# Performance work log

Hardware: AMD Instinct MI355X
Metric: run time of the kernel (lower is better)

The kernel has to match this reference:

```python
import jax, jax.numpy as jnp
import numpy as np

D = 384      # d_model
DM = 256     # memory feature dim
DF = 1536    # dim_feedforward
EPS = 1e-5


def _layer_norm(x, g, b):
    m = jnp.mean(x, axis=-1, keepdims=True)
    v = jnp.mean(jnp.square(x - m), axis=-1, keepdims=True)
    return (x - m) * jax.lax.rsqrt(v + EPS) * g + b


def setup_inputs() -> dict:
    key = jax.random.key(0)
    ks = jax.random.split(key, 24)
    B, T, T1, Tc = 8, 2048, 2048, 2048
    s = 0.02
    inp = {
        "tgt": jax.random.normal(ks[0], (B, T, D), jnp.float32),
        "memory": jax.random.normal(ks[1], (B, T1, DM), jnp.float32),
        "a1": jnp.float32(0.5),
        "score_c": jax.random.normal(ks[2], (B, 1, Tc, T1), jnp.float32) * 0.1,
        "out_c": jax.random.normal(ks[3], (B, Tc, D), jnp.float32),
        # attention projections
        "Wq": jax.random.normal(ks[4], (D, D), jnp.float32) * s,
        "bq": jnp.zeros((D,), jnp.float32),
        "Wk": jax.random.normal(ks[5], (DM, D), jnp.float32) * s,
        "bk": jnp.zeros((D,), jnp.float32),
        "Wv": jax.random.normal(ks[6], (DM, D), jnp.float32) * s,
        "bv": jnp.zeros((D,), jnp.float32),
        "Wu": jax.random.normal(ks[7], (D, D), jnp.float32) * s,  # unknown
        "bu": jnp.zeros((D,), jnp.float32),
        "Wn": jax.random.normal(ks[8], (D, D), jnp.float32) * s,  # known
        "bn": jnp.zeros((D,), jnp.float32),
        # FFN
        "W1": jax.random.normal(ks[9], (D, DF), jnp.float32) * s,
        "b1": jnp.zeros((DF,), jnp.float32),
        "W2": jax.random.normal(ks[10], (DF, D), jnp.float32) * s,
        "b2": jnp.zeros((D,), jnp.float32),
        # LayerNorms
        "g1": jnp.ones((D,), jnp.float32),
        "be1": jnp.zeros((D,), jnp.float32),
        "g2": jnp.ones((D,), jnp.float32),
        "be2": jnp.zeros((D,), jnp.float32),
    }
    return inp


def reference(tgt, memory, a1, score_c, out_c,
              Wq, bq, Wk, bk, Wv, bv, Wu, bu, Wn, bn,
              W1, b1, W2, b2, g1, be1, g2, be2):
    # --- En_De_Attention (n_head = 1; dropout p=0 / eval mode -> identity) ---
    scale = 1.0 / jnp.sqrt(jnp.float32(D))
    q = tgt @ Wq + bq                  # [B,T,D]
    k = memory @ Wk + bk               # [B,T1,D]
    v = memory @ Wv + bv               # [B,T1,D]
    att = jnp.einsum('btd,bsd->bts', q, k) * scale            # [B,T,T1]

    unknow = tgt @ Wu + bu             # [B,T,D]
    know = out_c @ Wn + bn             # [B,Tc,D]
    score1 = jnp.einsum('btd,bcd->btc', unknow, know) * scale  # [B,T,Tc]
    mixed = jnp.einsum('btc,bcs->bts', score1, score_c[:, 0])  # [B,T,T1]

    # tt = a1 in (0,1]: blended-score branch of the original module
    score = a1 * jax.nn.softmax(mixed, axis=-1) \
          + (1.0 - a1) * jax.nn.softmax(att, axis=-1)          # [B,T,T1]
    z = jnp.einsum('bts,bsd->btd', score, v)                   # [B,T,D]

    # --- residual + norm1 ---
    x = _layer_norm(tgt + z, g1, be1)
    # --- FFN (relu) + residual + norm2 (dropout eval -> identity) ---
    ff = jax.nn.relu(x @ W1 + b1) @ W2 + b2
    out = _layer_norm(x + ff, g2, be2)
    # score2 returned with head dim, matching torch shape [B,1,T,T1]
    return out, score[:, None]
```

## Files before the change

### kernel.cpp

```cpp
#include <hip/hip_runtime.h>
#include <stdint.h>

typedef __attribute__((ext_vector_type(8))) short bf16x8;
typedef __attribute__((ext_vector_type(4))) float f32x4;

__device__ __forceinline__ short f2bf(float f) {
    union { float f; unsigned u; } v; v.f = f;
    unsigned r = v.u + 0x7fffu + ((v.u >> 16) & 1u);
    return (short)(r >> 16);
}
__device__ __forceinline__ float bf2f(short s) {
    union { unsigned u; float f; } v;
    v.u = ((unsigned)(unsigned short)s) << 16;
    return v.f;
}

__device__ __forceinline__ void gld16(const void* g, void* l) {
    auto gp = reinterpret_cast<const __attribute__((address_space(1))) unsigned int*>(
        reinterpret_cast<uintptr_t>(g));
    auto lp = reinterpret_cast<__attribute__((address_space(3))) unsigned int*>(
        reinterpret_cast<uintptr_t>(l));
    __builtin_amdgcn_global_load_lds(gp, lp, 16, 0, 0);
}

template<int OUTBF, int BIASMODE , int DORELU>
__global__ __launch_bounds__(256, 3) void gemm128r(
    const short* __restrict__ Ag, const short* __restrict__ Bg,
    void* __restrict__ Cg, const float* __restrict__ bias,
    int K, int lda, int ldb, int ldc,
    long long sA, long long sB, long long sC,
    long long dA, long long dB, long long dC, float scale)
{
    __shared__ short lds[3 * 8192];
    const int t = threadIdx.x;
    const int lane = t & 63;
    const int wave = t >> 6;
    const int wm = wave >> 1, wn = wave & 1;

    const int gx = gridDim.x, gy = gridDim.y;
    const int nwg = gx * gy * gridDim.z;
    int id = blockIdx.x + gx * (blockIdx.y + gy * blockIdx.z);
    id = (id & 7) * (nwg >> 3) + (id >> 3);
    const int bx = id % gx;
    const int by = (id / gx) % gy;
    const int bz = id / (gx * gy);
    const int zlo = bz & 7, zhi = bz >> 3;

    const long long row0 = (long long)by * 128;
    const long long col0 = (long long)bx * 128;
    const int NT = K >> 5;

    const int gk = ((t & 3) ^ ((t >> 2) & 3) ^ ((t >> 4) & 3)) * 8;
    const short* Asrc = Ag + zlo * sA + zhi * dA + (row0 + (t >> 2)) * (long long)lda + gk;
    const short* Bsrc = Bg + zlo * sB + zhi * dB + (col0 + (t >> 2)) * (long long)ldb + gk;

    const int frow = lane & 15;
    const int fcol = ((lane >> 4) ^ (frow & 3) ^ ((frow >> 2) & 3)) * 8;

    f32x4 acc[4][4] = {};

#define STG(BUF, KC) do { \
        gld16(Asrc + (KC), &lds[(BUF) * 8192 + t * 8]); \
        gld16(Asrc + (KC) + 64LL * lda, &lds[(BUF) * 8192 + 2048 + t * 8]); \
        gld16(Bsrc + (KC), &lds[(BUF) * 8192 + 4096 + t * 8]); \
        gld16(Bsrc + (KC) + 64LL * ldb, &lds[(BUF) * 8192 + 6144 + t * 8]); } while (0)

    STG(0, 0);
    STG(1, 32);
    asm volatile("s_waitcnt vmcnt(4)\ns_barrier" ::: "memory");

    for (int kt = 0; kt < NT; ++kt) {
        const int rb = (kt % 3) * 8192;
        bf16x8 av[4], bv[4];
#pragma unroll
        for (int m = 0; m < 4; ++m)
            av[m] = *(const bf16x8*)&lds[rb + (wm * 64 + m * 16 + frow) * 32 + fcol];
#pragma unroll
        for (int n = 0; n < 4; ++n)
            bv[n] = *(const bf16x8*)&lds[rb + 4096 + (wn * 64 + n * 16 + frow) * 32 + fcol];
        if (kt + 2 < NT) STG((kt + 2) % 3, (long long)(kt + 2) * 32);
        __builtin_amdgcn_s_setprio(1);
#pragma unroll
        for (int m = 0; m < 4; ++m)
#pragma unroll
            for (int n = 0; n < 4; ++n)
                acc[m][n] = __builtin_amdgcn_mfma_f32_16x16x32_bf16(av[m], bv[n], acc[m][n], 0, 0, 0);
        __builtin_amdgcn_s_setprio(0);
        if (kt + 1 < NT) {
            if (kt + 2 < NT) asm volatile("s_waitcnt vmcnt(4)\ns_barrier" ::: "memory");
            else             asm volatile("s_waitcnt vmcnt(0)\ns_barrier" ::: "memory");
        }
    }
#undef STG

    const int crow = (lane >> 4) * 4;
    const int ccol = lane & 15;
    const long long cz = zlo * sC + zhi * dC;
#pragma unroll
    for (int m = 0; m < 4; ++m)
#pragma unroll
        for (int n = 0; n < 4; ++n)
#pragma unroll
            for (int i = 0; i < 4; ++i) {
                long long r = row0 + wm * 64 + m * 16 + crow + i;
                long long c = col0 + wn * 64 + n * 16 + ccol;
                float v = acc[m][n][i] * scale;
                if (BIASMODE == 1) v += bias[c];
                if (BIASMODE == 2) v += bias[r];
                if (DORELU) v = fmaxf(v, 0.0f);
                long long idx = cz + r * (long long)ldc + c;
                if (OUTBF) ((short*)Cg)[idx] = f2bf(v);
                else ((float*)Cg)[idx] = v;
            }
}

#define RD_A(RB, M, KS) (*(const bf16x8*)&lds[(RB) + (wm * 64 + (M) * 16 + frow) * 64 + \
        ((((KS) << 2) | fq) ^ (frow & 7)) * 8])
#define RD_B(RB, Nn, KS) (*(const bf16x8*)&lds[(RB) + 8192 + (wn * 64 + (Nn) * 16 + frow) * 64 + \
        ((((KS) << 2) | fq) ^ (frow & 7)) * 8])

__global__ __launch_bounds__(256, 2) void gemm128pz(
    const short* __restrict__ A1, const short* __restrict__ B1, short* __restrict__ C1,
    const float* __restrict__ bias1, int K1, int lda1, int ldb1, int ldc1,
    long long sB1, long long sC1,
    const short* __restrict__ A2, const short* __restrict__ B2, short* __restrict__ C2,
    const float* __restrict__ bias2, int K2, int lda2, int ldb2, int ldc2,
    long long sB2, long long sC2)
{
    __shared__ short lds[2 * 16384];
    const int t = threadIdx.x;
    const int lane = t & 63;
    const int wave = t >> 6;
    const int wm = wave >> 1, wn = wave & 1;

    const int gx = gridDim.x, gy = gridDim.y;
    const int nwg = gx * gy * gridDim.z;
    int id = blockIdx.x + gx * (blockIdx.y + gy * blockIdx.z);
    id = (id & 7) * (nwg >> 3) + (id >> 3);
    const int bx = id % gx;
    const int by = (id / gx) % gy;
    const int bz = id / (gx * gy);

    const bool sel = bz >= 8;
    const int zz = bz & 7;
    const short* Ag = sel ? A2 : A1;
    const short* Bg = sel ? B2 : B1;
    short* Cg = sel ? C2 : C1;
    const float* bias = sel ? bias2 : bias1;
    const int K = sel ? K2 : K1;
    const int lda = sel ? lda2 : lda1;
    const int ldb = sel ? ldb2 : ldb1;
    const int ldc = sel ? ldc2 : ldc1;
    const long long sB = sel ? sB2 : sB1;
    const long long sC = sel ? sC2 : sC1;

    const long long row0 = (long long)by * 128;
    const long long col0 = (long long)bx * 128;
    const int NT = K >> 6;

    const int srow = t >> 3;
    const int gk = ((t & 7) ^ (srow & 7)) * 8;
    const short* Asrc = Ag + (row0 + srow) * (long long)lda + gk;
    const short* Bsrc = Bg + (long long)zz * sB + (col0 + srow) * (long long)ldb + gk;

    const int frow = lane & 15;
    const int fq = lane >> 4;

    f32x4 acc[4][4] = {};

#define STAGE_A(WB, KC) do { _Pragma("unroll") \
        for (int r = 0; r < 4; ++r) \
            gld16(Asrc + (KC) + (long long)r * 32 * lda, &lds[(WB) + t * 8 + r * 2048]); } while (0)
#define STAGE_B(WB, KC) do { _Pragma("unroll") \
        for (int r = 0; r < 4; ++r) \
            gld16(Bsrc + (KC) + (long long)r * 32 * ldb, &lds[(WB) + 8192 + t * 8 + r * 2048]); } while (0)

    STAGE_A(0, 0);
    STAGE_B(0, 0);
    asm volatile("s_waitcnt vmcnt(0)\ns_barrier" ::: "memory");

    for (int kt = 0; kt < NT; ++kt) {
        const int rb = (kt & 1) << 14;
        const int wb = ((kt + 1) & 1) << 14;
        const bool st = (kt + 1) < NT;
        const long long kc = (long long)(kt + 1) << 6;

        bf16x8 av[4], bv[4];

#pragma unroll
        for (int m = 0; m < 4; ++m) av[m] = RD_A(rb, m, 0);
#pragma unroll
        for (int n = 0; n < 4; ++n) bv[n] = RD_B(rb, n, 0);
        if (st) STAGE_A(wb, kc);
        asm volatile("s_barrier" ::: "memory");
        __builtin_amdgcn_s_setprio(1);
#pragma unroll
        for (int m = 0; m < 4; ++m)
#pragma unroll
            for (int n = 0; n < 4; ++n)
                acc[m][n] = __builtin_amdgcn_mfma_f32_16x16x32_bf16(av[m], bv[n], acc[m][n], 0, 0, 0);
        __builtin_amdgcn_s_setprio(0);
        asm volatile("s_barrier" ::: "memory");

#pragma unroll
        for (int m = 0; m < 4; ++m) av[m] = RD_A(rb, m, 1);
#pragma unroll
        for (int n = 0; n < 4; ++n) bv[n] = RD_B(rb, n, 1);
        if (st) STAGE_B(wb, kc);
        asm volatile("s_barrier" ::: "memory");
        __builtin_amdgcn_s_setprio(1);
#pragma unroll
        for (int m = 0; m < 4; ++m)
#pragma unroll
            for (int n = 0; n < 4; ++n)
                acc[m][n] = __builtin_amdgcn_mfma_f32_16x16x32_bf16(av[m], bv[n], acc[m][n], 0, 0, 0);
        __builtin_amdgcn_s_setprio(0);
        if (st) asm volatile("s_waitcnt vmcnt(0)\ns_barrier" ::: "memory");
        else    asm volatile("s_barrier" ::: "memory");
    }
#undef STAGE_A
#undef STAGE_B

    const int crow = (lane >> 4) * 4;
    const int ccol = lane & 15;
    const long long cz = (long long)zz * sC;
#pragma unroll
    for (int m = 0; m < 4; ++m)
#pragma unroll
        for (int n = 0; n < 4; ++n)
#pragma unroll
            for (int i = 0; i < 4; ++i) {
                long long r = row0 + wm * 64 + m * 16 + crow + i;
                long long c = col0 + wn * 64 + n * 16 + ccol;
                float v = acc[m][n][i] + bias[r];
                Cg[cz + r * (long long)ldc + c] = f2bf(v);
            }
}
#undef RD_A
#undef RD_B

__global__ __launch_bounds__(256) void cast_all(
    const float* __restrict__ tgt, const float* __restrict__ mem, const float* __restrict__ outc,
    const float* __restrict__ bq, const float* __restrict__ bu,
    short* __restrict__ tgtb, short* __restrict__ memb, short* __restrict__ outcb,
    float* __restrict__ qubias)
{
    const long long R1 = 1572864;
    const long long R2 = R1 + 1048576;
    const long long R3 = R2 + 1572864;
    const long long R4 = R3 + 192;
    long long i = (long long)blockIdx.x * 256 + threadIdx.x;
    const float* in; short* out; long long j;
    if (i < R1) { in = tgt; out = tgtb; j = i; }
    else if (i < R2) { in = mem; out = memb; j = i - R1; }
    else if (i < R3) { in = outc; out = outcb; j = i - R2; }
    else if (i < R4) {
        j = i - R3;
        ((float4*)qubias)[j] = (j < 96) ? ((const float4*)bq)[j] : ((const float4*)bu)[j - 96];
        return;
    } else return;
    float4 v = ((const float4*)in)[j];
    short4 o;
    o.x = f2bf(v.x); o.y = f2bf(v.y); o.z = f2bf(v.z); o.w = f2bf(v.w);
    ((short4*)out)[j] = o;
}

__global__ __launch_bounds__(256) void transpose_all(
    const float* __restrict__ Wq, const float* __restrict__ Wk, const float* __restrict__ Wv,
    const float* __restrict__ Wu, const float* __restrict__ Wn,
    const float* __restrict__ W1, const float* __restrict__ W2,
    short* __restrict__ WquT, short* __restrict__ WkT, short* __restrict__ WvT,
    short* __restrict__ WnT, short* __restrict__ W1T, short* __restrict__ W2T)
{
    __shared__ float tile[64][65];
    int b = blockIdx.x;
    const float* in; short* out; int R, C, local;
    if (b < 36)       { in = Wq; out = WquT;          R = 384;  C = 384;  local = b; }
    else if (b < 60)  { in = Wk; out = WkT;           R = 256;  C = 384;  local = b - 36; }
    else if (b < 84)  { in = Wv; out = WvT;           R = 256;  C = 384;  local = b - 60; }
    else if (b < 120) { in = Wu; out = WquT + 147456; R = 384;  C = 384;  local = b - 84; }
    else if (b < 156) { in = Wn; out = WnT;           R = 384;  C = 384;  local = b - 120; }
    else if (b < 300) { in = W1; out = W1T;           R = 384;  C = 1536; local = b - 156; }
    else              { in = W2; out = W2T;           R = 1536; C = 384;  local = b - 300; }
    const int nbx = C >> 6;
    const int r0 = (local / nbx) * 64, c0 = (local % nbx) * 64;
    const int lr = threadIdx.x >> 6, lc = threadIdx.x & 63;
#pragma unroll
    for (int i = 0; i < 16; ++i) {
        int r = lr * 16 + i;
        tile[r][lc] = in[(long long)(r0 + r) * C + c0 + lc];
    }
    __syncthreads();
#pragma unroll
    for (int i = 0; i < 16; ++i) {
        int r = lr * 16 + i;
        out[(long long)(c0 + r) * R + r0 + lc] = f2bf(tile[lc][r]);
    }
}

__global__ __launch_bounds__(256) void transpose_cast(
    const float* __restrict__ in, short* __restrict__ out,
    int R, int C, long long sIn, long long sOut)
{
    __shared__ float tile[64][65];
    const long long zi = (long long)blockIdx.z * sIn;
    const long long zo = (long long)blockIdx.z * sOut;
    const int r0 = blockIdx.y * 64, c0 = blockIdx.x * 64;
    const int lr = threadIdx.x >> 6, lc = threadIdx.x & 63;
#pragma unroll
    for (int i = 0; i < 16; ++i) {
        int r = lr * 16 + i;
        tile[r][lc] = in[zi + (long long)(r0 + r) * C + c0 + lc];
    }
    __syncthreads();
#pragma unroll
    for (int i = 0; i < 16; ++i) {
        int r = lr * 16 + i;
        out[zo + (long long)(c0 + r) * R + r0 + lc] = f2bf(tile[lc][r]);
    }
}

__global__ __launch_bounds__(256) void softmax_blend(
    const short* __restrict__ attb, const short* __restrict__ mixb,
    const float* __restrict__ a1p,
    float* __restrict__ outF, short* __restrict__ outB)
{
    const int S = 2048;
    const long long row = blockIdx.x;
    const short* ar = attb + row * S;
    const short* mr = mixb + row * S;
    const int t = threadIdx.x;
    const int wave = t >> 6;

    bf16x8 a8 = *(const bf16x8*)&ar[t * 8];
    bf16x8 m8 = *(const bf16x8*)&mr[t * 8];
    float av[8], mv[8];
#pragma unroll
    for (int i = 0; i < 8; ++i) { av[i] = bf2f(a8[i]); mv[i] = bf2f(m8[i]); }

    float amax = av[0], mmax = mv[0];
#pragma unroll
    for (int i = 1; i < 8; ++i) { amax = fmaxf(amax, av[i]); mmax = fmaxf(mmax, mv[i]); }
#pragma unroll
    for (int o = 32; o; o >>= 1) {
        amax = fmaxf(amax, __shfl_xor(amax, o));
        mmax = fmaxf(mmax, __shfl_xor(mmax, o));
    }
    __shared__ float red[2][4];
    if ((t & 63) == 0) { red[0][wave] = amax; red[1][wave] = mmax; }
    __syncthreads();
    amax = fmaxf(fmaxf(red[0][0], red[0][1]), fmaxf(red[0][2], red[0][3]));
    mmax = fmaxf(fmaxf(red[1][0], red[1][1]), fmaxf(red[1][2], red[1][3]));

    float asum = 0.f, msum = 0.f;
#pragma unroll
    for (int i = 0; i < 8; ++i) {
        av[i] = __expf(av[i] - amax); asum += av[i];
        mv[i] = __expf(mv[i] - mmax); msum += mv[i];
    }
#pragma unroll
    for (int o = 32; o; o >>= 1) {
        asum += __shfl_xor(asum, o);
        msum += __shfl_xor(msum, o);
    }
    __shared__ float red2[2][4];
    if ((t & 63) == 0) { red2[0][wave] = asum; red2[1][wave] = msum; }
    __syncthreads();
    asum = red2[0][0] + red2[0][1] + red2[0][2] + red2[0][3];
    msum = red2[1][0] + red2[1][1] + red2[1][2] + red2[1][3];

    const float a1 = a1p[0];
    const float wm = a1 / msum;
    const float wa = (1.0f - a1) / asum;

    float o0[8];
    bf16x8 ob;
#pragma unroll
    for (int i = 0; i < 8; ++i) {
        float s = wm * mv[i] + wa * av[i];
        o0[i] = s;
        ob[i] = f2bf(s);
    }
    float4 f0, f1;
    f0.x = o0[0]; f0.y = o0[1]; f0.z = o0[2]; f0.w = o0[3];
    f1.x = o0[4]; f1.y = o0[5]; f1.z = o0[6]; f1.w = o0[7];
    *(float4*)&outF[row * S + t * 8] = f0;
    *(float4*)&outF[row * S + t * 8 + 4] = f1;
    *(bf16x8*)&outB[row * S + t * 8] = ob;
}

template<int WRITE_BF>
__global__ __launch_bounds__(256) void ln_kernel(
    const float* __restrict__ X, const float* __restrict__ Yr,
    const float* __restrict__ g, const float* __restrict__ be,
    float* __restrict__ outF, short* __restrict__ outB)
{
    const int Dm = 384;
    const int wave = threadIdx.x >> 6, lane = threadIdx.x & 63;
    const long long row = (long long)blockIdx.x * 4 + wave;
    const float* x = X + row * Dm;
    const float* y = Yr + row * Dm;
    float h[6];
    float s = 0.f, s2 = 0.f;
#pragma unroll
    for (int j = 0; j < 6; ++j) {
        int c = j * 64 + lane;
        h[j] = x[c] + y[c];
        s += h[j]; s2 += h[j] * h[j];
    }
#pragma unroll
    for (int o = 32; o; o >>= 1) { s += __shfl_xor(s, o); s2 += __shfl_xor(s2, o); }
    const float mean = s * (1.0f / 384.0f);
    const float var = s2 * (1.0f / 384.0f) - mean * mean;
    const float rstd = rsqrtf(var + 1e-5f);
#pragma unroll
    for (int j = 0; j < 6; ++j) {
        int c = j * 64 + lane;
        float v = (h[j] - mean) * rstd * g[c] + be[c];
        outF[row * Dm + c] = v;
        if (WRITE_BF) outB[row * Dm + c] = f2bf(v);
    }
}

extern "C" void kernel_launch(void* const* d_in, const int* in_sizes, int n_in,
                              void* d_out, int out_size, void* d_ws, size_t ws_size,
                              hipStream_t stream) {
    const float* tgt     = (const float*)d_in[0];
    const float* memory  = (const float*)d_in[1];
    const float* a1      = (const float*)d_in[2];
    const float* score_c = (const float*)d_in[3];
    const float* out_c   = (const float*)d_in[4];
    const float* Wq = (const float*)d_in[5];  const float* bq = (const float*)d_in[6];
    const float* Wk = (const float*)d_in[7];  const float* bk = (const float*)d_in[8];
    const float* Wv = (const float*)d_in[9];  const float* bv = (const float*)d_in[10];
    const float* Wu = (const float*)d_in[11]; const float* bu = (const float*)d_in[12];
    const float* Wn = (const float*)d_in[13]; const float* bn = (const float*)d_in[14];
    const float* W1 = (const float*)d_in[15]; const float* b1 = (const float*)d_in[16];
    const float* W2 = (const float*)d_in[17]; const float* b2 = (const float*)d_in[18];
    const float* g1 = (const float*)d_in[19]; const float* be1 = (const float*)d_in[20];
    const float* g2 = (const float*)d_in[21]; const float* be2 = (const float*)d_in[22];

    const long long BT = 16384;
    const long long S2 = 2048LL * 2048;
    const long long PB = 2048LL * 384;
    char* ws = (char*)d_ws;
    size_t off = 0;
    auto A_ = [&](size_t b) { size_t r = off; off += (b + 255) & ~(size_t)255; return r; };

    const size_t oTgtB  = A_(BT * 384 * 2);
    const size_t oMemB  = A_(BT * 256 * 2);
    const size_t oOutcB = A_(BT * 384 * 2);
    const size_t oWquT  = A_(768 * 384 * 2);
    const size_t oWnT   = A_(384 * 384 * 2);
    const size_t oWkT   = A_(384 * 256 * 2);
    const size_t oWvT   = A_(384 * 256 * 2);
    const size_t oW1T   = A_(1536 * 384 * 2);
    const size_t oW2T   = A_(384 * 1536 * 2);
    const size_t oQUb   = A_(768 * 4);
    const size_t oQU    = A_(16 * PB * 2);
    const size_t oKP    = A_(16 * PB * 2);
    const size_t oVT    = A_(8LL * 384 * 2048 * 2);
    const size_t oJ     = A_(8 * S2 * 2);
    const size_t oKr    = A_(8 * S2 * 2);
    const size_t oAM    = A_(16 * S2 * 2);
    const size_t oX     = A_(BT * 384 * 4);
    const size_t oXB    = A_(BT * 384 * 2);

    short* tgt_bf  = (short*)(ws + oTgtB);
    short* mem_bf  = (short*)(ws + oMemB);
    short* outc_bf = (short*)(ws + oOutcB);
    short* WquT = (short*)(ws + oWquT);
    short* WnT  = (short*)(ws + oWnT);
    short* WkT  = (short*)(ws + oWkT);
    short* WvT  = (short*)(ws + oWvT);
    short* W1T  = (short*)(ws + oW1T);
    short* W2T  = (short*)(ws + oW2T);
    float* qu_bias = (float*)(ws + oQUb);
    short* qu_bf  = (short*)(ws + oQU);
    short* k_bf   = (short*)(ws + oKP);
    short* Pt_bf  = k_bf + 8 * PB;
    short* vT_bf  = (short*)(ws + oVT);
    short* score_bf = (short*)(ws + oJ);
    short* scoreCt  = (short*)(ws + oKr);
    float* z_f      = (float*)(ws + oKr);
    short* knoT_bf  = (short*)(ws + oAM);
    short* att_bf   = (short*)(ws + oAM);
    short* mix_bf   = att_bf + 8 * S2;
    short* h_bf     = (short*)(ws + oAM);
    float* ff_f     = (float*)(ws + oAM + 8 * S2 * 2);
    float* x_f  = (float*)(ws + oX);
    short* x_bf = (short*)(ws + oXB);

    float* outMain = (float*)d_out;
    float* outScore = (float*)d_out + 6291456;

    const float SC = 0.05103103630798288f;
    dim3 blk(256);

    cast_all<<<16385, blk, 0, stream>>>(tgt, memory, out_c, bq, bu,
                                        tgt_bf, mem_bf, outc_bf, qu_bias);
    transpose_all<<<444, blk, 0, stream>>>(Wq, Wk, Wv, Wu, Wn, W1, W2,
                                           WquT, WkT, WvT, WnT, W1T, W2T);
    transpose_cast<<<dim3(32, 32, 8), blk, 0, stream>>>(score_c, scoreCt, 2048, 2048, S2, S2);

    gemm128r<1, 1, 0><<<dim3(6, 128, 1), blk, 0, stream>>>(
        tgt_bf, WquT, qu_bf, qu_bias, 384, 384, 384, 768, 0, 0, 0, 0, 0, 0, 1.0f);
    gemm128r<1, 1, 0><<<dim3(3, 128, 1), blk, 0, stream>>>(
        mem_bf, WkT, k_bf, bk, 256, 256, 256, 384, 0, 0, 0, 0, 0, 0, 1.0f);
    gemm128pz<<<dim3(16, 3, 16), blk, 0, stream>>>(
        WvT, mem_bf, vT_bf, bv, 256, 256, 256, 2048, 2048LL * 256, PB,
        WnT, outc_bf, knoT_bf, bn, 384, 384, 384, 2048, PB, PB);
    gemm128r<1, 0, 0><<<dim3(3, 16, 8), blk, 0, stream>>>(
        scoreCt, knoT_bf, Pt_bf, nullptr, 2048, 2048, 2048, 384,
        S2, PB, PB, 0, 0, 0, 1.0f);
    gemm128r<1, 0, 0><<<dim3(16, 16, 16), blk, 0, stream>>>(
        qu_bf, k_bf, att_bf, nullptr, 384, 768, 384, 2048,
        2048LL * 768, PB, S2, 384, 8 * PB, 8 * S2, SC);
    softmax_blend<<<16384, blk, 0, stream>>>(att_bf, mix_bf, a1, outScore, score_bf);
    gemm128r<0, 0, 0><<<dim3(3, 16, 8), blk, 0, stream>>>(
        score_bf, vT_bf, z_f, nullptr, 2048, 2048, 2048, 384,
        S2, PB, PB, 0, 0, 0, 1.0f);
    ln_kernel<1><<<4096, blk, 0, stream>>>(tgt, z_f, g1, be1, x_f, x_bf);
    gemm128r<1, 1, 1><<<dim3(12, 128, 1), blk, 0, stream>>>(
        x_bf, W1T, h_bf, b1, 384, 384, 384, 1536, 0, 0, 0, 0, 0, 0, 1.0f);
    gemm128r<0, 1, 0><<<dim3(3, 128, 1), blk, 0, stream>>>(
        h_bf, W2T, ff_f, b2, 1536, 1536, 1536, 384, 0, 0, 0, 0, 0, 0, 1.0f);
    ln_kernel<0><<<4096, blk, 0, stream>>>(x_f, ff_f, g2, be2, outMain, nullptr);
}
```

Before: 456.3 us.

## Add 128x256 wide-tile GEMM and split-K the score·V GEMM

Measured after the change: 866.8 us. 1.9x slower.

```diff
diff --git a/kernel.cpp b/kernel.cpp
--- a/kernel.cpp
+++ b/kernel.cpp
@@ -21,6 +21,98 @@
     auto lp = reinterpret_cast<__attribute__((address_space(3))) unsigned int*>(
         reinterpret_cast<uintptr_t>(l));
     __builtin_amdgcn_global_load_lds(gp, lp, 16, 0, 0);
+}
+
+template<int OUTBF, int BIASMODE , int DORELU>
+__global__ __launch_bounds__(256, 2) void gemmWide(
+    const short* __restrict__ Ag, const short* __restrict__ Bg,
+    void* __restrict__ Cg, const float* __restrict__ bias,
+    int K, int lda, int ldb, int ldc,
+    long long sA, long long sB, long long sC,
+    long long dA, long long dB, long long dC, float scale)
+{
+    __shared__ short lds[3 * 12288];
+    const int t = threadIdx.x;
+    const int lane = t & 63;
+    const int wave = t >> 6;
+    const int wm = wave >> 1, wn = wave & 1;
+
+    const int gx = gridDim.x, gy = gridDim.y;
+    const int nwg = gx * gy * gridDim.z;
+    int id = blockIdx.x + gx * (blockIdx.y + gy * blockIdx.z);
+    id = (id & 7) * (nwg >> 3) + (id >> 3);
+    const int bx = id % gx;
+    const int by = (id / gx) % gy;
+    const int bz = id / (gx * gy);
+    const int zlo = bz & 7, zhi = bz >> 3;
+
+    const long long row0 = (long long)by * 128;
+    const long long col0 = (long long)bx * 256;
+    const int NT = K >> 5;
+
+    const int gk = ((t & 3) ^ ((t >> 2) & 3) ^ ((t >> 4) & 3)) * 8;
+    const short* Asrc = Ag + zlo * sA + zhi * dA + (row0 + (t >> 2)) * (long long)lda + gk;
+    const short* Bsrc = Bg + zlo * sB + zhi * dB + (col0 + (t >> 2)) * (long long)ldb + gk;
+
+    const int frow = lane & 15;
+    const int fcol = ((lane >> 4) ^ (frow & 3) ^ ((frow >> 2) & 3)) * 8;
+
+    f32x4 acc[4][8] = {};
+
+#define STG(BUF, KC) do { \
+        gld16(Asrc + (KC), &lds[(BUF) * 12288 + t * 8]); \
+        gld16(Asrc + (KC) + 64LL * lda, &lds[(BUF) * 12288 + 2048 + t * 8]); \
+        gld16(Bsrc + (KC), &lds[(BUF) * 12288 + 4096 + t * 8]); \
+        gld16(Bsrc + (KC) + 64LL * ldb, &lds[(BUF) * 12288 + 6144 + t * 8]); \
+        gld16(Bsrc + (KC) + 128LL * ldb, &lds[(BUF) * 12288 + 8192 + t * 8]); \
+        gld16(Bsrc + (KC) + 192LL * ldb, &lds[(BUF) * 12288 + 10240 + t * 8]); } while (0)
+
+    STG(0, 0);
+    STG(1, 32);
+    asm volatile("s_waitcnt vmcnt(6)\ns_barrier" ::: "memory");
+
+    for (int kt = 0; kt < NT; ++kt) {
+        const int rb = (kt % 3) * 12288;
+        bf16x8 av[4], bv[8];
+#pragma unroll
+        for (int m = 0; m < 4; ++m)
+            av[m] = *(const bf16x8*)&lds[rb + (wm * 64 + m * 16 + frow) * 32 + fcol];
+#pragma unroll
+        for (int n = 0; n < 8; ++n)
+            bv[n] = *(const bf16x8*)&lds[rb + 4096 + (wn * 128 + n * 16 + frow) * 32 + fcol];
+        if (kt + 2 < NT) STG((kt + 2) % 3, (long long)(kt + 2) * 32);
+        __builtin_amdgcn_s_setprio(1);
+#pragma unroll
+        for (int m = 0; m < 4; ++m)
+#pragma unroll
+            for (int n = 0; n < 8; ++n)
+                acc[m][n] = __builtin_amdgcn_mfma_f32_16x16x32_bf16(av[m], bv[n], acc[m][n], 0, 0, 0);
+        __builtin_amdgcn_s_setprio(0);
+        if (kt + 1 < NT) {
+            if (kt + 2 < NT) asm volatile("s_waitcnt vmcnt(6)\ns_barrier" ::: "memory");
+            else             asm volatile("s_waitcnt vmcnt(0)\ns_barrier" ::: "memory");
+        }
+    }
+#undef STG
+
+    const int crow = (lane >> 4) * 4;
+    const int ccol = lane & 15;
+    const long long cz = zlo * sC + zhi * dC;
+#pragma unroll
+    for (int m = 0; m < 4; ++m)
+#pragma unroll
+        for (int n = 0; n < 8; ++n)
+#pragma unroll
+            for (int i = 0; i < 4; ++i) {
+                long long r = row0 + wm * 64 + m * 16 + crow + i;
+                long long c = col0 + wn * 128 + n * 16 + ccol;
+                float v = acc[m][n][i] * scale;
+                if (BIASMODE == 1) v += bias[c];
+                if (DORELU) v = fmaxf(v, 0.0f);
+                long long idx = cz + r * (long long)ldc + c;
+                if (OUTBF) ((short*)Cg)[idx] = f2bf(v);
+                else ((float*)Cg)[idx] = v;
+            }
 }
 
 template<int OUTBF, int BIASMODE , int DORELU>
@@ -389,9 +481,10 @@
     *(bf16x8*)&outB[row * S + t * 8] = ob;
 }
 
-template<int WRITE_BF>
+template<int WRITE_BF, int TWO_Y>
 __global__ __launch_bounds__(256) void ln_kernel(
     const float* __restrict__ X, const float* __restrict__ Yr,
+    const float* __restrict__ Y2,
     const float* __restrict__ g, const float* __restrict__ be,
     float* __restrict__ outF, short* __restrict__ outB)
 {
@@ -400,12 +493,14 @@
     const long long row = (long long)blockIdx.x * 4 + wave;
     const float* x = X + row * Dm;
     const float* y = Yr + row * Dm;
+    const float* y2 = TWO_Y ? (Y2 + row * Dm) : nullptr;
     float h[6];
     float s = 0.f, s2 = 0.f;
 #pragma unroll
     for (int j = 0; j < 6; ++j) {
         int c = j * 64 + lane;
         h[j] = x[c] + y[c];
+        if (TWO_Y) h[j] += y2[c];
         s += h[j]; s2 += h[j] * h[j];
     }
 #pragma unroll
@@ -482,7 +577,8 @@
     short* vT_bf  = (short*)(ws + oVT);
     short* score_bf = (short*)(ws + oJ);
     short* scoreCt  = (short*)(ws + oKr);
-    float* z_f      = (float*)(ws + oKr);
+    float* z0_f     = (float*)(ws + oKr);
+    float* z1_f     = z0_f + 6291456;
     short* knoT_bf  = (short*)(ws + oAM);
     short* att_bf   = (short*)(ws + oAM);
     short* mix_bf   = att_bf + 8 * S2;
@@ -503,7 +599,7 @@
                                            WquT, WkT, WvT, WnT, W1T, W2T);
     transpose_cast<<<dim3(32, 32, 8), blk, 0, stream>>>(score_c, scoreCt, 2048, 2048, S2, S2);
 
-    gemm128r<1, 1, 0><<<dim3(6, 128, 1), blk, 0, stream>>>(
+    gemmWide<1, 1, 0><<<dim3(3, 128, 1), blk, 0, stream>>>(
         tgt_bf, WquT, qu_bf, qu_bias, 384, 384, 384, 768, 0, 0, 0, 0, 0, 0, 1.0f);
     gemm128r<1, 1, 0><<<dim3(3, 128, 1), blk, 0, stream>>>(
         mem_bf, WkT, k_bf, bk, 256, 256, 256, 384, 0, 0, 0, 0, 0, 0, 1.0f);
@@ -513,17 +609,17 @@
     gemm128r<1, 0, 0><<<dim3(3, 16, 8), blk, 0, stream>>>(
         scoreCt, knoT_bf, Pt_bf, nullptr, 2048, 2048, 2048, 384,
         S2, PB, PB, 0, 0, 0, 1.0f);
-    gemm128r<1, 0, 0><<<dim3(16, 16, 16), blk, 0, stream>>>(
+    gemmWide<1, 0, 0><<<dim3(8, 128, 16), blk, 0, stream>>>(
         qu_bf, k_bf, att_bf, nullptr, 384, 768, 384, 2048,
         2048LL * 768, PB, S2, 384, 8 * PB, 8 * S2, SC);
     softmax_blend<<<16384, blk, 0, stream>>>(att_bf, mix_bf, a1, outScore, score_bf);
-    gemm128r<0, 0, 0><<<dim3(3, 16, 8), blk, 0, stream>>>(
-        score_bf, vT_bf, z_f, nullptr, 2048, 2048, 2048, 384,
-        S2, PB, PB, 0, 0, 0, 1.0f);
-    ln_kernel<1><<<4096, blk, 0, stream>>>(tgt, z_f, g1, be1, x_f, x_bf);
-    gemm128r<1, 1, 1><<<dim3(12, 128, 1), blk, 0, stream>>>(
+    gemm128r<0, 0, 0><<<dim3(3, 16, 16), blk, 0, stream>>>(
+        score_bf, vT_bf, z0_f, nullptr, 1024, 2048, 2048, 384,
+        S2, PB, PB, 1024, 1024, 6291456, 1.0f);
+    ln_kernel<1, 1><<<4096, blk, 0, stream>>>(tgt, z0_f, z1_f, g1, be1, x_f, x_bf);
+    gemmWide<1, 1, 1><<<dim3(6, 128, 1), blk, 0, stream>>>(
         x_bf, W1T, h_bf, b1, 384, 384, 384, 1536, 0, 0, 0, 0, 0, 0, 1.0f);
     gemm128r<0, 1, 0><<<dim3(3, 128, 1), blk, 0, stream>>>(
         h_bf, W2T, ff_f, b2, 1536, 1536, 1536, 384, 0, 0, 0, 0, 0, 0, 1.0f);
-    ln_kernel<0><<<4096, blk, 0, stream>>>(x_f, ff_f, g2, be2, outMain, nullptr);
-}
+    ln_kernel<0, 0><<<4096, blk, 0, stream>>>(x_f, ff_f, nullptr, g2, be2, outMain, nullptr);
+}
```
